# Performance work log

Measured on AMD Instinct MI355X. Metric: run time of the kernel, lower is better.

The kernel has to match this reference:

```python
import jax, jax.numpy as jnp
import numpy as np

N_E = 512
E_DIM = 128
LEGACY = 0.2
B, T = 64, 1024


def setup_inputs() -> dict:
    key = jax.random.key(0)
    k1, k2 = jax.random.split(key, 2)
    key_soft = jax.random.normal(k1, (B, T, E_DIM), dtype=jnp.float32)
    emb_weight = jax.random.uniform(k2, (N_E + 1, E_DIM), dtype=jnp.float32,
                                    minval=-1.0 / N_E, maxval=1.0 / N_E)
    zero_ts_mask = jnp.zeros((B,), dtype=jnp.bool_)
    return {"key_soft": key_soft, "emb_weight": emb_weight, "zero_ts_mask": zero_ts_mask}


def _neighbor_indices(d, zero_ts_mask, n_e):
    # d: [B, T, n_e+1] (no grad needed; only used for int index selection)
    ind0 = jnp.clip(jnp.argmin(d[:, 0, :], axis=1), 0, n_e - 1)
    ind0 = jnp.where(zero_ts_mask, 0, ind0)

    def step(ind, d_t):  # ind: [B], d_t: [B, n_e+1]
        d_here = jnp.take_along_axis(d_t, ind[:, None], axis=1)[:, 0]
        ind_next = jnp.clip(ind + 1, 0, n_e - 1)
        d_next = jnp.take_along_axis(d_t, ind_next[:, None], axis=1)[:, 0]
        ind_new = jnp.where(d_here <= d_next, ind, ind_next)
        return ind_new, ind_new

    _, rest = jax.lax.scan(step, ind0, jnp.swapaxes(d[:, 1:, :], 0, 1))  # [T-1, B]
    return jnp.concatenate([ind0[None, :], rest], axis=0).T  # [B, T]


def reference(key_soft, emb_weight, zero_ts_mask):
    sg = jax.lax.stop_gradient
    n_e = emb_weight.shape[0] - 1
    b, t, e_dim = key_soft.shape

    # squared-distance matrix: [B, T, n_e+1]
    d = (jnp.sum(key_soft ** 2, axis=-1, keepdims=True)
         + jnp.sum(emb_weight ** 2, axis=1)
         - 2.0 * jnp.einsum('btd,nd->btn', key_soft, emb_weight))
    d_ng = sg(d)

    min_indices = jnp.argmin(d_ng, axis=-1)                 # [B, T] (over full n_e+1)
    enc = _neighbor_indices(d_ng, zero_ts_mask, n_e)        # [B, T]

    key_hard_here = emb_weight[enc]                                  # [B, T, D]
    key_hard_next = emb_weight[jnp.clip(enc + 1, 0, n_e - 1)]        # [B, T, D]
    key_min = emb_weight[min_indices]                                # [B, T, D]

    def vq_loss(kh):
        return (jnp.sum((sg(key_soft) - kh) ** 2, axis=-1)
                + jnp.sum((key_soft - sg(kh)) ** 2, axis=-1) * LEGACY)

    loss_here_base = vq_loss(key_hard_here)
    loss_next_base = vq_loss(key_hard_next)

    energy = (jnp.sum((sg(key_soft) - key_hard_next) ** 2, axis=-1)
              - jnp.sum((sg(key_soft) - key_hard_here) ** 2, axis=-1)
              + (jnp.sum((key_soft - sg(key_hard_next)) ** 2, axis=-1)
                 - jnp.sum((key_soft - sg(key_hard_here)) ** 2, axis=-1)) * LEGACY)

    change = (enc[:, 1:] - enc[:, :-1]) != 0
    same_hard_mask = jnp.where(change, 0.0, 1.0)
    energy_change = (energy[:, 1:] - energy[:, :-1]) * same_hard_mask
    loss_energy_descent = jnp.maximum(energy_change + 1e-06 / n_e,
                                      jnp.zeros_like(energy_change)).mean()
    energy_mean = energy.mean()

    loss_min_indices = vq_loss(key_min)
    loss_min_here = jnp.where(loss_min_indices < loss_here_base, loss_min_indices, 0.0)
    loss_min_next = jnp.where(loss_min_indices < loss_next_base, loss_min_indices, 0.0)

    loss_here = loss_here_base - loss_next_base - loss_min_here
    loss_next = loss_next_base - loss_here_base - loss_min_next

    key_hard = key_soft + sg(key_hard_here - key_soft)  # straight-through

    v = jnp.max(jnp.max(enc, axis=1) - jnp.min(enc, axis=1))
    return (key_hard, enc, v, loss_here, loss_next, energy_mean, loss_energy_descent)
```

## Files before the change

kernel.cpp:

```cpp
#include <hip/hip_runtime.h>
#include <cfloat>
#include <cstdint>

#define B_  64
#define T_  1024
#define D_  128
#define NE  512
#define P_  (B_*T_)

#define O_KH   0
#define O_ENC  (P_*D_)
#define O_V    (O_ENC + P_)
#define O_LH   (O_V + 1)
#define O_LN   (O_LH + P_)
#define O_EM   (O_LN + P_)
#define O_LED  (O_EM + 1)

typedef __attribute__((ext_vector_type(8))) short bf16x8;
typedef __attribute__((ext_vector_type(4))) float floatx4;
typedef unsigned long long u64;

__device__ __forceinline__ void pack8(const float4& a, const float4& b,
                                      uint4& h, uint4& l)
{
    float v[8] = {a.x,a.y,a.z,a.w,b.x,b.y,b.z,b.w};
    unsigned hw[4], lw[4];
    #pragma unroll
    for (int e = 0; e < 4; e++) {
        const unsigned ua = __float_as_uint(v[2*e]);
        const unsigned ub = __float_as_uint(v[2*e+1]);
        const float fa = __uint_as_float(ua & 0xffff0000u);
        const float fb = __uint_as_float(ub & 0xffff0000u);
        const unsigned da = __float_as_uint(v[2*e]   - fa);
        const unsigned db = __float_as_uint(v[2*e+1] - fb);
        hw[e] = (ub & 0xffff0000u) | (ua >> 16);
        lw[e] = (db & 0xffff0000u) | (da >> 16);
    }
    h = make_uint4(hw[0],hw[1],hw[2],hw[3]);
    l = make_uint4(lw[0],lw[1],lw[2],lw[3]);
}

__device__ __forceinline__ u64 shflx64(u64 v, int d)
{
    const int lo = __shfl_xor((int)(unsigned)(v & 0xffffffffULL), d);
    const int hi = __shfl_xor((int)(unsigned)(v >> 32), d);
    return ((u64)(unsigned)hi << 32) | (unsigned)lo;
}

__device__ __forceinline__ unsigned sortkey(float f)
{
    const unsigned b = __float_as_uint(f);
    return b ^ (unsigned)(((int)b >> 31) | (int)0x80000000);
}

__global__ __launch_bounds__(256) void kFG(const float* __restrict__ emb,
                                           unsigned short* __restrict__ ehi,
                                           unsigned short* __restrict__ elo,
                                           float* __restrict__ sq,
                                           unsigned* __restrict__ cnt)
{
    if (blockIdx.x == 0 && threadIdx.x == 0) *cnt = 0u;
    const int t = blockIdx.x * 256 + threadIdx.x;
    const int n = t >> 2, kst = t & 3;
    const float4* src = (const float4*)(emb + (size_t)n * D_ + kst * 32);
    float ss = 0.f;
    #pragma unroll
    for (int g = 0; g < 4; g++) {
        const float4 a = src[2*g], b = src[2*g+1];
        ss += a.x*a.x + a.y*a.y + a.z*a.z + a.w*a.w
            + b.x*b.x + b.y*b.y + b.z*b.z + b.w*b.w;
        uint4 h, l;
        pack8(a, b, h, l);
        const int f = ((n >> 4) * 4 + kst) * 4 + g;
        *(uint4*)(ehi + (size_t)f*128 + (size_t)(n & 15)*8) = h;
        *(uint4*)(elo + (size_t)f*128 + (size_t)(n & 15)*8) = l;
    }
    ss += __shfl_xor(ss, 1);
    ss += __shfl_xor(ss, 2);
    if (kst == 0) sq[n] = ss;
}

__global__ __launch_bounds__(512, 4) void kA(const float* __restrict__ ks,
                                          const float* __restrict__ sq,
                                          const unsigned short* __restrict__ ehi,
                                          const unsigned short* __restrict__ elo,
                                          u64* __restrict__ bits,
                                          float* __restrict__ sfirst,
                                          float* __restrict__ slast,
                                          unsigned* __restrict__ mins,
                                          unsigned short* __restrict__ mini16)
{
    __shared__ unsigned short Bh[32*128];
    __shared__ unsigned short Bl[32*128];

    const int tid  = threadIdx.x;
    const int lane = tid & 63;
    const int wv   = tid >> 6;
    const int m    = lane & 15;
    const int q    = lane >> 4;
    const int bid  = blockIdx.x;
    const int h    = bid >> 10;
    const int pt   = bid & 1023;
    const int p0   = pt * 64 + h * 32;
    const int ch   = wv;
    const int nb   = ch * 64;

    {
        const int srow = tid >> 4;
        const int scg  = tid & 15;
        const float4* sp = (const float4*)(ks + ((size_t)p0 + srow)*D_ + scg*8);
        uint4 hh, ll;
        pack8(sp[0], sp[1], hh, ll);
        const int cb = (srow*256 + scg*16) ^ ((srow & 7) << 4);
        *(uint4*)((char*)Bh + cb) = hh;
        *(uint4*)((char*)Bl + cb) = ll;
    }
    __syncthreads();

    floatx4 acc[4][2];
    #pragma unroll
    for (int i = 0; i < 4; i++)
        #pragma unroll
        for (int j = 0; j < 2; j++)
            #pragma unroll
            for (int r = 0; r < 4; r++) acc[i][j][r] = 0.f;

    bf16x8 ah[4], al[4], bh[2], bl[2];

    auto loadA = [&](int kst) {
        #pragma unroll
        for (int i = 0; i < 4; i++) {
            const int off = (((ch*4 + i) * 4 + kst) * 4 + q) * 128 + m*8;
            ah[i] = *(const bf16x8*)(ehi + off);
            al[i] = *(const bf16x8*)(elo + off);
        }
    };
    auto loadB = [&](int kst) {
        #pragma unroll
        for (int j = 0; j < 2; j++) {
            const int row = j*16 + m;
            const int cb = (row*256 + kst*64 + q*16) ^ ((row & 7) << 4);
            bh[j] = *(const bf16x8*)((const char*)Bh + cb);
            bl[j] = *(const bf16x8*)((const char*)Bl + cb);
        }
    };
    auto mfma3 = [&]() {
        __builtin_amdgcn_s_setprio(1);
        #pragma unroll
        for (int i = 0; i < 4; i++)
            #pragma unroll
            for (int j = 0; j < 2; j++)
                acc[i][j] = __builtin_amdgcn_mfma_f32_16x16x32_bf16(ah[i], bh[j], acc[i][j], 0, 0, 0);
        #pragma unroll
        for (int i = 0; i < 4; i++)
            #pragma unroll
            for (int j = 0; j < 2; j++)
                acc[i][j] = __builtin_amdgcn_mfma_f32_16x16x32_bf16(ah[i], bl[j], acc[i][j], 0, 0, 0);
        #pragma unroll
        for (int i = 0; i < 4; i++)
            #pragma unroll
            for (int j = 0; j < 2; j++)
                acc[i][j] = __builtin_amdgcn_mfma_f32_16x16x32_bf16(al[i], bh[j], acc[i][j], 0, 0, 0);
        __builtin_amdgcn_s_setprio(0);
    };

    #pragma unroll
    for (int kst = 0; kst < 3; kst++) {
        loadA(kst);
        loadB(kst);
        mfma3();
    }
    loadA(3);
    loadB(3);
    float sa[4][4];
    #pragma unroll
    for (int i = 0; i < 4; i++) {
        const float4 s4 = *(const float4*)(sq + nb + i*16 + q*4);
        sa[i][0]=s4.x; sa[i][1]=s4.y; sa[i][2]=s4.z; sa[i][3]=s4.w;
    }
    mfma3();

    #pragma unroll
    for (int j = 0; j < 2; j++) {
        float S[4][4];
        #pragma unroll
        for (int i = 0; i < 4; i++)
            #pragma unroll
            for (int r = 0; r < 4; r++)
                S[i][r] = fmaf(-2.f, acc[i][j][r], sa[i][r]);

        float nq[4], ni[4];
        #pragma unroll
        for (int i = 0; i < 4; i++) nq[i] = __shfl_down(S[i][0], 16);
        #pragma unroll
        for (int i = 0; i < 3; i++) ni[i] = __shfl(S[i+1][0], m);
        ni[3] = 0.f;

        u64 w = 0;
        #pragma unroll
        for (int i = 0; i < 4; i++) {
            #pragma unroll
            for (int r = 0; r < 3; r++)
                w |= (u64)(S[i][r] <= S[i][r+1]) << (16*i + 4*q + r);
            if (!(i == 3 && q == 3)) {
                const float nxt = (q < 3) ? nq[i] : ni[i];
                w |= (u64)(S[i][3] <= nxt) << (16*i + 4*q + 3);
            }
        }
        if (ch == 7 && q == 3) w |= 1ULL << 63;
        w |= shflx64(w, 16);
        w |= shflx64(w, 32);

        float mv = S[0][0]; int mi_ = nb + q*4;
        #pragma unroll
        for (int i = 0; i < 4; i++)
            #pragma unroll
            for (int r = 0; r < 4; r++) {
                if (i == 0 && r == 0) continue;
                const int nid = nb + 16*i + 4*q + r;
                if (S[i][r] < mv) { mv = S[i][r]; mi_ = nid; }
            }
        #pragma unroll
        for (int d = 16; d <= 32; d <<= 1) {
            const float v2 = __shfl_xor(mv, d);
            const int   i2 = __shfl_xor(mi_, d);
            if (v2 < mv || (v2 == mv && i2 < mi_)) { mv = v2; mi_ = i2; }
        }

        const size_t pg = (size_t)(p0 + j*16 + m);
        if (q == 0) {
            bits  [pg*8 + ch] = w;
            sfirst[pg*8 + ch] = S[0][0];
            mins  [pg*8 + ch] = sortkey(mv);
            mini16[pg*8 + ch] = (unsigned short)mi_;
        }
        if (q == 3) slast[pg*8 + ch] = S[3][3];
    }
}

struct KBwin { u64 W[8]; float F[8]; float L[8]; };

__global__ __launch_bounds__(64) void kB(const float* __restrict__ ks,
                                         const float* __restrict__ emb,
                                         const unsigned char* __restrict__ mask,
                                         const u64* __restrict__ bits,
                                         const float* __restrict__ sfirst,
                                         const float* __restrict__ slast,
                                         const unsigned* __restrict__ mins,
                                         const unsigned short* __restrict__ mini16,
                                         int* __restrict__ enci,
                                         float* __restrict__ out)
{
    const int b    = blockIdx.x;
    const int lane = threadIdx.x;
    const size_t p0 = (size_t)b * T_;

    const float2 e = ((const float2*)(emb + (size_t)512*D_))[lane];
    const float2 k = ((const float2*)(ks  + p0*D_))[lane];
    float s5 = e.x*(e.x - 2.f*k.x) + e.y*(e.y - 2.f*k.y);
    #pragma unroll
    for (int m = 32; m >= 1; m >>= 1) s5 += __shfl_xor(s5, m);

    u64 kk = ~0ULL;
    if (lane < 8)       kk = ((u64)mins[p0*8 + lane] << 32) | (u64)mini16[p0*8 + lane];
    else if (lane == 8) kk = ((u64)sortkey(s5) << 32) | 512ULL;
    #pragma unroll
    for (int d = 1; d <= 8; d <<= 1) {
        const u64 o = shflx64(kk, d);
        kk = (o < kk) ? o : kk;
    }
    const int mi = __shfl((int)(unsigned)(kk & 0xffffffffULL), 0);
    int cur = (mi < NE) ? mi : NE - 1;
    if (mask[b]) cur = 0;
    if (lane == 0) { enci[p0] = cur; out[O_ENC + p0] = (float)cur; }

    KBwin wa, wb;

    auto loadwin = [&](KBwin& d, int t0) {
        const int t = t0 + lane;
        if (t < T_) {
            const ulonglong2* bp = (const ulonglong2*)(bits + (p0 + t)*8);
            const ulonglong2 w01 = bp[0], w23 = bp[1], w45 = bp[2], w67 = bp[3];
            d.W[0]=w01.x; d.W[1]=w01.y; d.W[2]=w23.x; d.W[3]=w23.y;
            d.W[4]=w45.x; d.W[5]=w45.y; d.W[6]=w67.x; d.W[7]=w67.y;
            const float4* fp = (const float4*)(sfirst + (p0 + t)*8);
            const float4 f0 = fp[0], f1 = fp[1];
            d.F[0]=f0.x; d.F[1]=f0.y; d.F[2]=f0.z; d.F[3]=f0.w;
            d.F[4]=f1.x; d.F[5]=f1.y; d.F[6]=f1.z; d.F[7]=f1.w;
            const float4* lp = (const float4*)(slast + (p0 + t)*8);
            const float4 l0 = lp[0], l1 = lp[1];
            d.L[0]=l0.x; d.L[1]=l0.y; d.L[2]=l0.z; d.L[3]=l0.w;
            d.L[4]=l1.x; d.L[5]=l1.y; d.L[6]=l1.z; d.L[7]=l1.w;
        } else {
            #pragma unroll
            for (int c = 0; c < 8; c++) { d.W[c] = ~0ULL; d.F[c] = 1.f; d.L[c] = 0.f; }
        }
    };

    auto scanwin = [&](KBwin& d, int t0) {
        #pragma unroll
        for (int c = 0; c < 7; c++)
            d.W[c] |= (u64)(d.L[c] <= d.F[c+1]) << 63;

        const int w0   = cur >> 6;
        const int off0 = cur & 63;
        u64 a = d.W[0];
        #pragma unroll
        for (int c = 1; c < 8; c++) a = (w0 == c) ? d.W[c] : a;
        u64 bn = ~0ULL;
        #pragma unroll
        for (int c = 1; c < 8; c++) bn = (w0 == c-1) ? d.W[c] : bn;
        const u64 u = (off0 == 0) ? a : ((a >> off0) | (bn << (64 - off0)));

        const unsigned ulo = (unsigned)u;
        const unsigned uhi = (unsigned)(u >> 32);
        int doff = 0;
        int myenc = cur;
        #pragma unroll
        for (int j = 0; j < 64; j++) {
            const unsigned slo = (unsigned)__builtin_amdgcn_readlane((int)ulo, j);
            const unsigned shi = (unsigned)__builtin_amdgcn_readlane((int)uhi, j);
            const u64 word = ((u64)shi << 32) | slo;
            const int bit = (int)((word >> doff) & 1ULL);
            doff += 1 - bit;
            if (lane == j) myenc = cur + doff;
        }
        cur += doff;
        const int t = t0 + lane;
        if (t < T_) {
            enci[p0 + t] = myenc;
            out[O_ENC + p0 + t] = (float)myenc;
        }
    };

    loadwin(wa, 1);
    #pragma unroll 1
    for (int wp = 0; wp < 8; wp++) {
        const int t0a = 1 + wp*128;
        loadwin(wb, t0a + 64);
        scanwin(wa, t0a);
        if (wp < 7) loadwin(wa, t0a + 128);
        scanwin(wb, t0a + 64);
    }
}

__global__ __launch_bounds__(256) void kC(const float* __restrict__ ks,
                                          const float* __restrict__ emb,
                                          const int* __restrict__ enci,
                                          const unsigned* __restrict__ mins,
                                          const unsigned short* __restrict__ mini16,
                                          float* __restrict__ out,
                                          float* __restrict__ energy)
{
    const int lane = threadIdx.x & 63;
    const size_t p = (size_t)blockIdx.x * 4 + (threadIdx.x >> 6);
    const int q  = lane >> 4;
    const int qm = lane & 15;

    const int eh = enci[p];
    const int en = (eh + 1 < NE) ? eh + 1 : NE - 1;
    const int row = (q == 0) ? eh : ((q == 1) ? en : 512);

    const float4* ksp = (const float4*)(ks + p*D_);
    const float4 k1 = ksp[qm*2], k2 = ksp[qm*2 + 1];
    const float4* ep = (const float4*)(emb + (size_t)row*D_);
    const float4 e1 = ep[qm*2], e2 = ep[qm*2 + 1];

    float d;
    if (q == 3) {
        d = k1.x*k1.x + k1.y*k1.y + k1.z*k1.z + k1.w*k1.w
          + k2.x*k2.x + k2.y*k2.y + k2.z*k2.z + k2.w*k2.w;
    } else {
        d = e1.x*(e1.x - 2.f*k1.x) + e1.y*(e1.y - 2.f*k1.y)
          + e1.z*(e1.z - 2.f*k1.z) + e1.w*(e1.w - 2.f*k1.w)
          + e2.x*(e2.x - 2.f*k2.x) + e2.y*(e2.y - 2.f*k2.y)
          + e2.z*(e2.z - 2.f*k2.z) + e2.w*(e2.w - 2.f*k2.w);
    }
    #pragma unroll
    for (int s = 1; s <= 8; s <<= 1) d += __shfl_xor(d, s);

    const float ph  = __shfl(d, 0);
    const float pn  = __shfl(d, 16);
    const float p5  = __shfl(d, 32);
    const float sqk = __shfl(d, 48);

    u64 kk = ~0ULL;
    if (lane < 8)       kk = ((u64)mins[p*8 + lane] << 32) | (u64)mini16[p*8 + lane];
    else if (lane == 8) kk = ((u64)sortkey(p5) << 32) | 512ULL;
    #pragma unroll
    for (int s = 1; s <= 8; s <<= 1) {
        const u64 o = shflx64(kk, s);
        kk = (o < kk) ? o : kk;
    }
    const int mi = __shfl((int)(unsigned)(kk & 0xffffffffULL), 0);

    float pm;
    if (mi == eh)      pm = ph;
    else if (mi == en) pm = pn;
    else if (mi == 512) pm = p5;
    else {
        const float4* mp = (const float4*)(emb + (size_t)mi*D_);
        const float4 m1 = mp[qm*2], m2 = mp[qm*2 + 1];
        float dm = m1.x*(m1.x - 2.f*k1.x) + m1.y*(m1.y - 2.f*k1.y)
                 + m1.z*(m1.z - 2.f*k1.z) + m1.w*(m1.w - 2.f*k1.w)
                 + m2.x*(m2.x - 2.f*k2.x) + m2.y*(m2.y - 2.f*k2.y)
                 + m2.z*(m2.z - 2.f*k2.z) + m2.w*(m2.w - 2.f*k2.w);
        #pragma unroll
        for (int s = 1; s <= 8; s <<= 1) dm += __shfl_xor(dm, s);
        pm = __shfl(dm, 0);
    }

    if (q == 0) {
        float4 o1, o2;
        o1.x = k1.x + (e1.x - k1.x); o1.y = k1.y + (e1.y - k1.y);
        o1.z = k1.z + (e1.z - k1.z); o1.w = k1.w + (e1.w - k1.w);
        o2.x = k2.x + (e2.x - k2.x); o2.y = k2.y + (e2.y - k2.y);
        o2.z = k2.z + (e2.z - k2.z); o2.w = k2.w + (e2.w - k2.w);
        ((float4*)(out + p*D_))[qm*2]     = o1;
        ((float4*)(out + p*D_))[qm*2 + 1] = o2;
    }

    if (lane == 0) {
        const float lh = 1.2f * (sqk + ph);
        const float ln = 1.2f * (sqk + pn);
        const float lm = 1.2f * (sqk + pm);
        out[O_LH + p] = lh - ln - ((pm < ph) ? lm : 0.f);
        out[O_LN + p] = ln - lh - ((pm < pn) ? lm : 0.f);
        energy[p] = 1.2f * (pn - ph);
    }
}

__global__ __launch_bounds__(256) void kD1(const float* __restrict__ energy,
                                           const int* __restrict__ enci,
                                           double2* __restrict__ part,
                                           unsigned* __restrict__ cnt,
                                           float* __restrict__ out)
{
    __shared__ double sA[256], sB[256];
    __shared__ unsigned done;
    const int p = blockIdx.x * 256 + threadIdx.x;
    const float e = energy[p];
    double se = (double)e;
    double sl = 0.0;
    if ((p & (T_-1)) < T_-1) {
        const float ec = (enci[p+1] == enci[p]) ? (energy[p+1] - e) : 0.f;
        sl = (double)fmaxf(ec + (float)(1e-6/512.0), 0.f);
    }
    sA[threadIdx.x] = se; sB[threadIdx.x] = sl;
    __syncthreads();
    for (int s = 128; s >= 1; s >>= 1) {
        if (threadIdx.x < (unsigned)s) {
            sA[threadIdx.x] += sA[threadIdx.x+s];
            sB[threadIdx.x] += sB[threadIdx.x+s];
        }
        __syncthreads();
    }
    if (threadIdx.x == 0) {
        part[blockIdx.x] = make_double2(sA[0], sB[0]);
        __threadfence();
        done = atomicAdd(cnt, 1u);
    }
    __syncthreads();
    if (done != 255u) return;

    __threadfence();
    double pvx, pvy;
    pvx = ((volatile double*)part)[2*threadIdx.x];
    pvy = ((volatile double*)part)[2*threadIdx.x + 1];
    __syncthreads();
    sA[threadIdx.x] = pvx; sB[threadIdx.x] = pvy;
    __syncthreads();
    for (int s = 128; s >= 1; s >>= 1) {
        if (threadIdx.x < (unsigned)s) {
            sA[threadIdx.x] += sA[threadIdx.x+s];
            sB[threadIdx.x] += sB[threadIdx.x+s];
        }
        __syncthreads();
    }
    if (threadIdx.x < 64) {
        int v = enci[(size_t)threadIdx.x*T_ + T_-1] - enci[(size_t)threadIdx.x*T_];
        #pragma unroll
        for (int m = 32; m >= 1; m >>= 1) {
            const int v2 = __shfl_xor(v, m);
            v = (v2 > v) ? v2 : v;
        }
        if (threadIdx.x == 0) {
            out[O_V]   = (float)v;
            out[O_EM]  = (float)(sA[0] / (double)P_);
            out[O_LED] = (float)(sB[0] / (double)(B_*(T_-1)));
        }
    }
}

extern "C" void kernel_launch(void* const* d_in, const int* in_sizes, int n_in,
                              void* d_out, int out_size, void* d_ws, size_t ws_size,
                              hipStream_t stream)
{
    const float* ks  = (const float*)d_in[0];
    const float* emb = (const float*)d_in[1];
    const unsigned char* mask = (const unsigned char*)d_in[2];

    float* out = (float*)d_out;
    char* w = (char*)d_ws;
    u64*      bits   = (u64*)     (w);
    float*    sfirst = (float*)   (w + (size_t) 4*1024*1024);
    float*    slast  = (float*)   (w + (size_t) 6*1024*1024);
    unsigned* mins   = (unsigned*)(w + (size_t) 8*1024*1024);
    unsigned short* mini16 = (unsigned short*)(w + (size_t)10*1024*1024);
    int*      enci   = (int*)     (w + (size_t)11*1024*1024);
    float*    energy = (float*)   (w + (size_t)11*1024*1024 + 256*1024);
    float*    sq     = (float*)   (w + (size_t)11*1024*1024 + 512*1024);
    double2*  part   = (double2*) (w + (size_t)11*1024*1024 + 516*1024);
    unsigned* cnt    = (unsigned*)(w + (size_t)11*1024*1024 + 520*1024);
    unsigned short* ehi = (unsigned short*)(w + (size_t)11*1024*1024 + 640*1024);
    unsigned short* elo = (unsigned short*)(w + (size_t)11*1024*1024 + 768*1024);

    kFG<<<8,    256, 0, stream>>>(emb, ehi, elo, sq, cnt);
    kA <<<2048, 512, 0, stream>>>(ks, sq, ehi, elo, bits, sfirst, slast, mins, mini16);
    kB <<<B_,   64,  0, stream>>>(ks, emb, mask, bits, sfirst, slast, mins, mini16, enci, out);
    kC <<<P_/4, 256, 0, stream>>>(ks, emb, enci, mins, mini16, out, energy);
    kD1<<<256,  256, 0, stream>>>(energy, enci, part, cnt, out);
}
```

Baseline: 182.5 us.

## Fuse per-batch scan into distance kernel via last-block atomic counter

Drops the separate scan kernel. Each distance block bumps a per-batch atomic counter, and the last of the 32 blocks for a batch runs the sequential neighbour scan on one wavefront. The A-operand loads are also double-buffered so the next k-step's loads overlap the current MFMAs. This removes a launch and lets scans for finished batches overlap other batches' distance work, at the cost of a thread fence, atomics, extra registers and a serial tail on the last block.

```diff
diff --git a/kernel.cpp b/kernel.cpp
--- a/kernel.cpp
+++ b/kernel.cpp
@@ -53,14 +53,18 @@
     return b ^ (unsigned)(((int)b >> 31) | (int)0x80000000);
 }
 
-__global__ __launch_bounds__(256) void kFG(const float* __restrict__ emb,
-                                           unsigned short* __restrict__ ehi,
-                                           unsigned short* __restrict__ elo,
-                                           float* __restrict__ sq,
-                                           unsigned* __restrict__ cnt)
-{
-    if (blockIdx.x == 0 && threadIdx.x == 0) *cnt = 0u;
-    const int t = blockIdx.x * 256 + threadIdx.x;
+__global__ __launch_bounds__(64) void kFG(const float* __restrict__ emb,
+                                          unsigned short* __restrict__ ehi,
+                                          unsigned short* __restrict__ elo,
+                                          float* __restrict__ sq,
+                                          unsigned* __restrict__ cnt,
+                                          unsigned* __restrict__ cntB)
+{
+    if (blockIdx.x == 0) {
+        cntB[threadIdx.x] = 0u;
+        if (threadIdx.x == 0) *cnt = 0u;
+    }
+    const int t = blockIdx.x * 64 + threadIdx.x;
     const int n = t >> 2, kst = t & 3;
     const float4* src = (const float4*)(emb + (size_t)n * D_ + kst * 32);
     float ss = 0.f;
@@ -80,179 +84,20 @@
     if (kst == 0) sq[n] = ss;
 }
 
-__global__ __launch_bounds__(512, 4) void kA(const float* __restrict__ ks,
-                                          const float* __restrict__ sq,
-                                          const unsigned short* __restrict__ ehi,
-                                          const unsigned short* __restrict__ elo,
-                                          u64* __restrict__ bits,
-                                          float* __restrict__ sfirst,
-                                          float* __restrict__ slast,
-                                          unsigned* __restrict__ mins,
-                                          unsigned short* __restrict__ mini16)
-{
-    __shared__ unsigned short Bh[32*128];
-    __shared__ unsigned short Bl[32*128];
-
-    const int tid  = threadIdx.x;
-    const int lane = tid & 63;
-    const int wv   = tid >> 6;
-    const int m    = lane & 15;
-    const int q    = lane >> 4;
-    const int bid  = blockIdx.x;
-    const int h    = bid >> 10;
-    const int pt   = bid & 1023;
-    const int p0   = pt * 64 + h * 32;
-    const int ch   = wv;
-    const int nb   = ch * 64;
-
-    {
-        const int srow = tid >> 4;
-        const int scg  = tid & 15;
-        const float4* sp = (const float4*)(ks + ((size_t)p0 + srow)*D_ + scg*8);
-        uint4 hh, ll;
-        pack8(sp[0], sp[1], hh, ll);
-        const int cb = (srow*256 + scg*16) ^ ((srow & 7) << 4);
-        *(uint4*)((char*)Bh + cb) = hh;
-        *(uint4*)((char*)Bl + cb) = ll;
-    }
-    __syncthreads();
-
-    floatx4 acc[4][2];
-    #pragma unroll
-    for (int i = 0; i < 4; i++)
-        #pragma unroll
-        for (int j = 0; j < 2; j++)
-            #pragma unroll
-            for (int r = 0; r < 4; r++) acc[i][j][r] = 0.f;
-
-    bf16x8 ah[4], al[4], bh[2], bl[2];
-
-    auto loadA = [&](int kst) {
-        #pragma unroll
-        for (int i = 0; i < 4; i++) {
-            const int off = (((ch*4 + i) * 4 + kst) * 4 + q) * 128 + m*8;
-            ah[i] = *(const bf16x8*)(ehi + off);
-            al[i] = *(const bf16x8*)(elo + off);
-        }
-    };
-    auto loadB = [&](int kst) {
-        #pragma unroll
-        for (int j = 0; j < 2; j++) {
-            const int row = j*16 + m;
-            const int cb = (row*256 + kst*64 + q*16) ^ ((row & 7) << 4);
-            bh[j] = *(const bf16x8*)((const char*)Bh + cb);
-            bl[j] = *(const bf16x8*)((const char*)Bl + cb);
-        }
-    };
-    auto mfma3 = [&]() {
-        __builtin_amdgcn_s_setprio(1);
-        #pragma unroll
-        for (int i = 0; i < 4; i++)
-            #pragma unroll
-            for (int j = 0; j < 2; j++)
-                acc[i][j] = __builtin_amdgcn_mfma_f32_16x16x32_bf16(ah[i], bh[j], acc[i][j], 0, 0, 0);
-        #pragma unroll
-        for (int i = 0; i < 4; i++)
-            #pragma unroll
-            for (int j = 0; j < 2; j++)
-                acc[i][j] = __builtin_amdgcn_mfma_f32_16x16x32_bf16(ah[i], bl[j], acc[i][j], 0, 0, 0);
-        #pragma unroll
-        for (int i = 0; i < 4; i++)
-            #pragma unroll
-            for (int j = 0; j < 2; j++)
-                acc[i][j] = __builtin_amdgcn_mfma_f32_16x16x32_bf16(al[i], bh[j], acc[i][j], 0, 0, 0);
-        __builtin_amdgcn_s_setprio(0);
-    };
-
-    #pragma unroll
-    for (int kst = 0; kst < 3; kst++) {
-        loadA(kst);
-        loadB(kst);
-        mfma3();
-    }
-    loadA(3);
-    loadB(3);
-    float sa[4][4];
-    #pragma unroll
-    for (int i = 0; i < 4; i++) {
-        const float4 s4 = *(const float4*)(sq + nb + i*16 + q*4);
-        sa[i][0]=s4.x; sa[i][1]=s4.y; sa[i][2]=s4.z; sa[i][3]=s4.w;
-    }
-    mfma3();
-
-    #pragma unroll
-    for (int j = 0; j < 2; j++) {
-        float S[4][4];
-        #pragma unroll
-        for (int i = 0; i < 4; i++)
-            #pragma unroll
-            for (int r = 0; r < 4; r++)
-                S[i][r] = fmaf(-2.f, acc[i][j][r], sa[i][r]);
-
-        float nq[4], ni[4];
-        #pragma unroll
-        for (int i = 0; i < 4; i++) nq[i] = __shfl_down(S[i][0], 16);
-        #pragma unroll
-        for (int i = 0; i < 3; i++) ni[i] = __shfl(S[i+1][0], m);
-        ni[3] = 0.f;
-
-        u64 w = 0;
-        #pragma unroll
-        for (int i = 0; i < 4; i++) {
-            #pragma unroll
-            for (int r = 0; r < 3; r++)
-                w |= (u64)(S[i][r] <= S[i][r+1]) << (16*i + 4*q + r);
-            if (!(i == 3 && q == 3)) {
-                const float nxt = (q < 3) ? nq[i] : ni[i];
-                w |= (u64)(S[i][3] <= nxt) << (16*i + 4*q + 3);
-            }
-        }
-        if (ch == 7 && q == 3) w |= 1ULL << 63;
-        w |= shflx64(w, 16);
-        w |= shflx64(w, 32);
-
-        float mv = S[0][0]; int mi_ = nb + q*4;
-        #pragma unroll
-        for (int i = 0; i < 4; i++)
-            #pragma unroll
-            for (int r = 0; r < 4; r++) {
-                if (i == 0 && r == 0) continue;
-                const int nid = nb + 16*i + 4*q + r;
-                if (S[i][r] < mv) { mv = S[i][r]; mi_ = nid; }
-            }
-        #pragma unroll
-        for (int d = 16; d <= 32; d <<= 1) {
-            const float v2 = __shfl_xor(mv, d);
-            const int   i2 = __shfl_xor(mi_, d);
-            if (v2 < mv || (v2 == mv && i2 < mi_)) { mv = v2; mi_ = i2; }
-        }
-
-        const size_t pg = (size_t)(p0 + j*16 + m);
-        if (q == 0) {
-            bits  [pg*8 + ch] = w;
-            sfirst[pg*8 + ch] = S[0][0];
-            mins  [pg*8 + ch] = sortkey(mv);
-            mini16[pg*8 + ch] = (unsigned short)mi_;
-        }
-        if (q == 3) slast[pg*8 + ch] = S[3][3];
-    }
-}
-
 struct KBwin { u64 W[8]; float F[8]; float L[8]; };
 
-__global__ __launch_bounds__(64) void kB(const float* __restrict__ ks,
-                                         const float* __restrict__ emb,
-                                         const unsigned char* __restrict__ mask,
-                                         const u64* __restrict__ bits,
-                                         const float* __restrict__ sfirst,
-                                         const float* __restrict__ slast,
-                                         const unsigned* __restrict__ mins,
-                                         const unsigned short* __restrict__ mini16,
-                                         int* __restrict__ enci,
-                                         float* __restrict__ out)
-{
-    const int b    = blockIdx.x;
-    const int lane = threadIdx.x;
+__device__ __forceinline__ void kb_scan(int b, int lane,
+                                        const float* __restrict__ ks,
+                                        const float* __restrict__ emb,
+                                        const unsigned char* __restrict__ mask,
+                                        const u64* __restrict__ bits,
+                                        const float* __restrict__ sfirst,
+                                        const float* __restrict__ slast,
+                                        const unsigned* __restrict__ mins,
+                                        const unsigned short* __restrict__ mini16,
+                                        int* __restrict__ enci,
+                                        float* __restrict__ out)
+{
     const size_t p0 = (size_t)b * T_;
 
     const float2 e = ((const float2*)(emb + (size_t)512*D_))[lane];
@@ -344,6 +189,179 @@
     }
 }
 
+__global__ __launch_bounds__(512, 4) void kA(const float* __restrict__ ks,
+                                          const float* __restrict__ emb,
+                                          const unsigned char* __restrict__ mask,
+                                          const float* __restrict__ sq,
+                                          const unsigned short* __restrict__ ehi,
+                                          const unsigned short* __restrict__ elo,
+                                          u64* __restrict__ bits,
+                                          float* __restrict__ sfirst,
+                                          float* __restrict__ slast,
+                                          unsigned* __restrict__ mins,
+                                          unsigned short* __restrict__ mini16,
+                                          unsigned* __restrict__ cntB,
+                                          int* __restrict__ enci,
+                                          float* __restrict__ out)
+{
+    __shared__ unsigned short Bh[32*128];
+    __shared__ unsigned short Bl[32*128];
+    __shared__ int isLast;
+
+    const int tid  = threadIdx.x;
+    const int lane = tid & 63;
+    const int wv   = tid >> 6;
+    const int m    = lane & 15;
+    const int q    = lane >> 4;
+    const int bid  = blockIdx.x;
+    const int h    = bid >> 10;
+    const int pt   = bid & 1023;
+    const int p0   = pt * 64 + h * 32;
+    const int ch   = wv;
+    const int nb   = ch * 64;
+
+    {
+        const int srow = tid >> 4;
+        const int scg  = tid & 15;
+        const float4* sp = (const float4*)(ks + ((size_t)p0 + srow)*D_ + scg*8);
+        uint4 hh, ll;
+        pack8(sp[0], sp[1], hh, ll);
+        const int cb = (srow*256 + scg*16) ^ ((srow & 7) << 4);
+        *(uint4*)((char*)Bh + cb) = hh;
+        *(uint4*)((char*)Bl + cb) = ll;
+    }
+    __syncthreads();
+
+    floatx4 acc[4][2];
+    #pragma unroll
+    for (int i = 0; i < 4; i++)
+        #pragma unroll
+        for (int j = 0; j < 2; j++)
+            #pragma unroll
+            for (int r = 0; r < 4; r++) acc[i][j][r] = 0.f;
+
+    bf16x8 ah0[4], al0[4], ah1[4], al1[4], bh[2], bl[2];
+
+    auto loadA = [&](int kst, bf16x8* AH, bf16x8* AL) {
+        #pragma unroll
+        for (int i = 0; i < 4; i++) {
+            const int off = (((ch*4 + i) * 4 + kst) * 4 + q) * 128 + m*8;
+            AH[i] = *(const bf16x8*)(ehi + off);
+            AL[i] = *(const bf16x8*)(elo + off);
+        }
+    };
+    auto loadB = [&](int kst) {
+        #pragma unroll
+        for (int j = 0; j < 2; j++) {
+            const int row = j*16 + m;
+            const int cb = (row*256 + kst*64 + q*16) ^ ((row & 7) << 4);
+            bh[j] = *(const bf16x8*)((const char*)Bh + cb);
+            bl[j] = *(const bf16x8*)((const char*)Bl + cb);
+        }
+    };
+    auto mfma3 = [&](const bf16x8* AH, const bf16x8* AL) {
+        __builtin_amdgcn_s_setprio(1);
+        #pragma unroll
+        for (int i = 0; i < 4; i++)
+            #pragma unroll
+            for (int j = 0; j < 2; j++)
+                acc[i][j] = __builtin_amdgcn_mfma_f32_16x16x32_bf16(AH[i], bh[j], acc[i][j], 0, 0, 0);
+        #pragma unroll
+        for (int i = 0; i < 4; i++)
+            #pragma unroll
+            for (int j = 0; j < 2; j++)
+                acc[i][j] = __builtin_amdgcn_mfma_f32_16x16x32_bf16(AH[i], bl[j], acc[i][j], 0, 0, 0);
+        #pragma unroll
+        for (int i = 0; i < 4; i++)
+            #pragma unroll
+            for (int j = 0; j < 2; j++)
+                acc[i][j] = __builtin_amdgcn_mfma_f32_16x16x32_bf16(AL[i], bh[j], acc[i][j], 0, 0, 0);
+        __builtin_amdgcn_s_setprio(0);
+    };
+
+    loadA(0, ah0, al0);
+    loadA(1, ah1, al1); loadB(0); mfma3(ah0, al0);
+    loadA(2, ah0, al0); loadB(1); mfma3(ah1, al1);
+    loadA(3, ah1, al1); loadB(2); mfma3(ah0, al0);
+    loadB(3);
+    float sa[4][4];
+    #pragma unroll
+    for (int i = 0; i < 4; i++) {
+        const float4 s4 = *(const float4*)(sq + nb + i*16 + q*4);
+        sa[i][0]=s4.x; sa[i][1]=s4.y; sa[i][2]=s4.z; sa[i][3]=s4.w;
+    }
+    mfma3(ah1, al1);
+
+    #pragma unroll
+    for (int j = 0; j < 2; j++) {
+        float S[4][4];
+        #pragma unroll
+        for (int i = 0; i < 4; i++)
+            #pragma unroll
+            for (int r = 0; r < 4; r++)
+                S[i][r] = fmaf(-2.f, acc[i][j][r], sa[i][r]);
+
+        float nq[4], ni[4];
+        #pragma unroll
+        for (int i = 0; i < 4; i++) nq[i] = __shfl_down(S[i][0], 16);
+        #pragma unroll
+        for (int i = 0; i < 3; i++) ni[i] = __shfl(S[i+1][0], m);
+        ni[3] = 0.f;
+
+        u64 w = 0;
+        #pragma unroll
+        for (int i = 0; i < 4; i++) {
+            #pragma unroll
+            for (int r = 0; r < 3; r++)
+                w |= (u64)(S[i][r] <= S[i][r+1]) << (16*i + 4*q + r);
+            if (!(i == 3 && q == 3)) {
+                const float nxt = (q < 3) ? nq[i] : ni[i];
+                w |= (u64)(S[i][3] <= nxt) << (16*i + 4*q + 3);
+            }
+        }
+        if (ch == 7 && q == 3) w |= 1ULL << 63;
+        w |= shflx64(w, 16);
+        w |= shflx64(w, 32);
+
+        float mv = S[0][0]; int mi_ = nb + q*4;
+        #pragma unroll
+        for (int i = 0; i < 4; i++)
+            #pragma unroll
+            for (int r = 0; r < 4; r++) {
+                if (i == 0 && r == 0) continue;
+                const int nid = nb + 16*i + 4*q + r;
+                if (S[i][r] < mv) { mv = S[i][r]; mi_ = nid; }
+            }
+        #pragma unroll
+        for (int d = 16; d <= 32; d <<= 1) {
+            const float v2 = __shfl_xor(mv, d);
+            const int   i2 = __shfl_xor(mi_, d);
+            if (v2 < mv || (v2 == mv && i2 < mi_)) { mv = v2; mi_ = i2; }
+        }
+
+        const size_t pg = (size_t)(p0 + j*16 + m);
+        if (q == 0) {
+            bits  [pg*8 + ch] = w;
+            sfirst[pg*8 + ch] = S[0][0];
+            mins  [pg*8 + ch] = sortkey(mv);
+            mini16[pg*8 + ch] = (unsigned short)mi_;
+        }
+        if (q == 3) slast[pg*8 + ch] = S[3][3];
+    }
+
+    const int b = pt >> 4;
+    __threadfence();
+    __syncthreads();
+    if (tid == 0) {
+        const unsigned old = atomicAdd(&cntB[b], 1u);
+        isLast = (old == 31u) ? 1 : 0;
+    }
+    __syncthreads();
+    if (!isLast || wv != 0) return;
+    __threadfence();
+    kb_scan(b, lane, ks, emb, mask, bits, sfirst, slast, mins, mini16, enci, out);
+}
+
 __global__ __launch_bounds__(256) void kC(const float* __restrict__ ks,
                                           const float* __restrict__ emb,
                                           const int* __restrict__ enci,
@@ -512,12 +530,13 @@
     float*    sq     = (float*)   (w + (size_t)11*1024*1024 + 512*1024);
     double2*  part   = (double2*) (w + (size_t)11*1024*1024 + 516*1024);
     unsigned* cnt    = (unsigned*)(w + (size_t)11*1024*1024 + 520*1024);
+    unsigned* cntB   = (unsigned*)(w + (size_t)11*1024*1024 + 524*1024);
     unsigned short* ehi = (unsigned short*)(w + (size_t)11*1024*1024 + 640*1024);
     unsigned short* elo = (unsigned short*)(w + (size_t)11*1024*1024 + 768*1024);
 
-    kFG<<<8,    256, 0, stream>>>(emb, ehi, elo, sq, cnt);
-    kA <<<2048, 512, 0, stream>>>(ks, sq, ehi, elo, bits, sfirst, slast, mins, mini16);
-    kB <<<B_,   64,  0, stream>>>(ks, emb, mask, bits, sfirst, slast, mins, mini16, enci, out);
+    kFG<<<32,   64,  0, stream>>>(emb, ehi, elo, sq, cnt, cntB);
+    kA <<<2048, 512, 0, stream>>>(ks, emb, mask, sq, ehi, elo, bits, sfirst, slast,
+                                  mins, mini16, cntB, enci, out);
     kC <<<P_/4, 256, 0, stream>>>(ks, emb, enci, mins, mini16, out, energy);
     kD1<<<256,  256, 0, stream>>>(energy, enci, part, cnt, out);
 }
```

After: 698.1 us. 3.83x slower.
